# Optimization experiments

Measured on AMD Instinct MI355X. Metric: run time of the kernel, lower is better.

The kernel has to match this reference:

```python
import jax, jax.numpy as jnp
import numpy as np

N_EMBD = 500
BLOCK_SIZE = 256


def _rope(q, k, theta=0.0001):
    # Faithful to the torch code: freq exponent uses the FULL dim C, and the
    # tensor is split into contiguous halves (not interleaved pairs).
    B, T, C = q.shape
    half = C // 2
    i = jnp.arange(half)
    freqs = theta ** (2.0 * (i // 2).astype(q.dtype) / C)  # [half]
    ang = jnp.arange(T, dtype=q.dtype)[:, None] * freqs[None, :]  # [T, half]
    cos_p, sin_p = jnp.cos(ang), jnp.sin(ang)
    q1, q2 = q[..., :half], q[..., half:]
    k1, k2 = k[..., :half], k[..., half:]
    q_rot = jnp.concatenate([q1 * cos_p - q2 * sin_p, q1 * sin_p + q2 * cos_p], axis=-1)
    k_rot = jnp.concatenate([k1 * cos_p - k2 * sin_p, k1 * sin_p + k2 * cos_p], axis=-1)
    return q_rot, k_rot


def setup_inputs() -> dict:
    key = jax.random.key(0)
    k1, k2, k3, k4 = jax.random.split(key, 4)
    B, T = 256, 256
    scale = 1.0 / np.sqrt(N_EMBD)
    x = jax.random.normal(k1, (B, T, N_EMBD), dtype=jnp.float32)
    Wq = jax.random.normal(k2, (N_EMBD, 500), dtype=jnp.float32) * scale
    Wk = jax.random.normal(k3, (N_EMBD, 500), dtype=jnp.float32) * scale
    Wv = jax.random.normal(k4, (N_EMBD, 500), dtype=jnp.float32) * scale
    return {"x": x, "Wq": Wq, "Wk": Wk, "Wv": Wv}


def reference(x, Wq, Wk, Wv):
    B, T, C = x.shape  # C == n_embd == 500
    q = jnp.einsum("btc,ch->bth", x, Wq)
    k = jnp.einsum("btc,ch->bth", x, Wk)
    q, k = _rope(q, k)
    # NOTE: original scales by input-dim C**-0.5 (500), not head_size**-0.5.
    wei = jnp.einsum("bth,bsh->bts", q, k) * (C ** -0.5)
    causal = jnp.tril(jnp.ones((T, T), dtype=bool))
    wei = jnp.where(causal, wei, -jnp.inf)
    wei = jax.nn.softmax(wei, axis=-1)
    # dropout: eval mode (identity) for deterministic reference
    v = jnp.einsum("btc,ch->bth", x, Wv)
    return jnp.einsum("bts,bsh->bth", wei, v)
```

## Files before the change

### kernel.cpp

```cpp
#include <hip/hip_runtime.h>

typedef unsigned short u16;
typedef __attribute__((ext_vector_type(8))) __bf16 bf16x8;
typedef __attribute__((ext_vector_type(4))) float f32x4;

__device__ __forceinline__ float bf2f(u16 u) {
  union { unsigned int i; float f; } v; v.i = ((unsigned int)u) << 16; return v.f;
}
__device__ __forceinline__ u16 f2bf(float f) {
  union { float f; unsigned int i; } v; v.f = f;
  unsigned int u = v.i;
  return (u16)((u + 0x7fffu + ((u >> 16) & 1u)) >> 16);
}
__device__ __forceinline__ void async16(void* lds, const void* g) {
  __builtin_amdgcn_global_load_lds(
      (const __attribute__((address_space(1))) unsigned int*)g,
      (__attribute__((address_space(3))) unsigned int*)lds, 16, 0, 0);
}

__global__ void k_convert_x(const float* __restrict__ x, u16* __restrict__ xb) {
  int idx = blockIdx.x * 256 + threadIdx.x;
  int m = idx >> 6, c0 = (idx & 63) * 8;
  u16 o[8];
  if (c0 < 496) {
    float4 v0 = *(const float4*)(x + (size_t)m * 500 + c0);
    float4 v1 = *(const float4*)(x + (size_t)m * 500 + c0 + 4);
    o[0] = f2bf(v0.x); o[1] = f2bf(v0.y); o[2] = f2bf(v0.z); o[3] = f2bf(v0.w);
    o[4] = f2bf(v1.x); o[5] = f2bf(v1.y); o[6] = f2bf(v1.z); o[7] = f2bf(v1.w);
  } else {
#pragma unroll
    for (int j = 0; j < 8; ++j) {
      int c = c0 + j;
      o[j] = f2bf((c < 500) ? x[(size_t)m * 500 + c] : 0.f);
    }
  }
  *(uint4*)(xb + (size_t)m * 512 + c0) = *(const uint4*)o;
}

__global__ void k_convert_w(const float* __restrict__ Wq, const float* __restrict__ Wk,
                            const float* __restrict__ Wv, u16* __restrict__ Wt) {
  int idx = blockIdx.x * 256 + threadIdx.x;
  int g = idx >> 18;
  int r = idx & 262143;
  int n = r >> 9, k = r & 511;
  const float* W = (g == 0) ? Wq : (g == 1) ? Wk : Wv;
  int orig = (g == 2) ? n : ((n & 1) ? (n >> 1) + 250 : (n >> 1));
  float v = (n < 500 && k < 500) ? W[(size_t)k * 500 + orig] : 0.f;
  Wt[idx] = f2bf(v);
}

__global__ void k_tables(float* __restrict__ cospair, float* __restrict__ sinpair) {
  int t = blockIdx.x, p = threadIdx.x;
  float c = 0.f, s = 0.f;
  if (p < 250) {
    float ex = (float)(2 * (p >> 1)) / 500.0f;
    float fr = powf(1e-4f, ex);
    float ang = (float)t * fr;
    c = cosf(ang); s = sinf(ang);
  }
  cospair[t * 256 + p] = c;
  sinpair[t * 256 + p] = s;
}

__global__ __launch_bounds__(512, 2) void k_gemm_qkv(
    const u16* __restrict__ xb, const u16* __restrict__ Wt,
    const float* __restrict__ cospair, const float* __restrict__ sinpair,
    u16* __restrict__ qb, u16* __restrict__ kb, u16* __restrict__ vT) {
  __shared__ u16 As[2][128][64];
  __shared__ u16 Bs[2][128][64];
  const int tid = threadIdx.x;
  const int lane = tid & 63;
  const int w = tid >> 6;
  const int wm = w >> 2, wn = w & 3;
  const int lrow = lane & 15, lhi = lane >> 4;
  const int sx = lrow & 7;

  int bid = blockIdx.x;
  int wk = (bid & 7) * 192 + (bid >> 3);
  int mg = wk / 12;
  int j12 = wk - mg * 12;
  int g = j12 >> 2, bni = j12 & 3;
  const int bn = bni << 7;
  const int m0 = mg << 9;

  const u16* Ab = xb + (size_t)m0 * 512;
  const u16* Bb = Wt + ((size_t)(g * 512 + bn)) * 512;

#define STAGE(S) { int mt_ = (S) >> 3, t_ = (S) & 7, buf_ = (S) & 1;          \
    _Pragma("unroll")                                                         \
    for (int ld = 0; ld < 2; ++ld) {                                          \
      int gi = ld * 512 + tid;                                                \
      int r_ = gi >> 3, c_ = gi & 7;                                          \
      int so_ = t_ * 64 + ((c_ ^ (r_ & 7)) * 8);                              \
      async16((char*)As + buf_ * 16384 + (size_t)gi * 16,                     \
              Ab + ((size_t)(mt_ * 128 + r_)) * 512 + so_);                   \
      async16((char*)Bs + buf_ * 16384 + (size_t)gi * 16,                     \
              Bb + (size_t)r_ * 512 + so_);                                   \
    } }

#define EPILOGUE(MT) {                                                        \
    int mb = m0 + (MT) * 128;                                                 \
    if (g < 2) {                                                              \
      u16* dst = (g == 0) ? qb : kb;                                          \
      _Pragma("unroll")                                                       \
      for (int mi = 0; mi < 4; ++mi)                                          \
        _Pragma("unroll")                                                     \
        for (int ni = 0; ni < 2; ++ni) {                                      \
          int n = bn + wn * 32 + ni * 16 + lrow;                              \
          int p = n >> 1;                                                     \
          _Pragma("unroll")                                                   \
          for (int jj = 0; jj < 4; ++jj) {                                    \
            int m = mb + wm * 64 + mi * 16 + lhi * 4 + jj;                    \
            float v = acc[mi][ni][jj];                                        \
            float o = __shfl_xor(v, 1, 64);                                   \
            int ti = (m & 255) * 256 + p;                                     \
            float c = cospair[ti], s = sinpair[ti];                           \
            float r = (n & 1) ? (o * s + v * c) : (v * c - o * s);            \
            dst[(size_t)m * 512 + n] = f2bf(r);                               \
          }                                                                   \
        }                                                                     \
    } else {                                                                  \
      _Pragma("unroll")                                                       \
      for (int mi = 0; mi < 4; ++mi)                                          \
        _Pragma("unroll")                                                     \
        for (int ni = 0; ni < 2; ++ni) {                                      \
          int n = bn + wn * 32 + ni * 16 + lrow;                              \
          _Pragma("unroll")                                                   \
          for (int jj = 0; jj < 4; ++jj) {                                    \
            int m = mb + wm * 64 + mi * 16 + lhi * 4 + jj;                    \
            vT[(size_t)(m >> 8) * 131072 + (size_t)n * 256 + (m & 255)] =     \
                f2bf(acc[mi][ni][jj]);                                        \
          }                                                                   \
        }                                                                     \
    } }

  STAGE(0);
  asm volatile("s_waitcnt vmcnt(0)" ::: "memory");
  __builtin_amdgcn_s_barrier();
  asm volatile("" ::: "memory");

  for (int mt = 0; mt < 4; ++mt) {
    f32x4 acc[4][2] = {};
#pragma unroll
    for (int t = 0; t < 8; ++t) {
      const int S = mt * 8 + t;
      if (S + 1 < 32) STAGE(S + 1);
      const u16* Asl = (const u16*)As + (t & 1) * 8192;
      const u16* Bsl = (const u16*)Bs + (t & 1) * 8192;
      bf16x8 a[4][2], bfr[2][2];
#pragma unroll
      for (int mi = 0; mi < 4; ++mi)
#pragma unroll
        for (int kk2 = 0; kk2 < 2; ++kk2)
          a[mi][kk2] = *(const bf16x8*)(Asl + (wm * 64 + mi * 16 + lrow) * 64 +
                                        (((kk2 * 4 + lhi) ^ sx) * 8));
#pragma unroll
      for (int ni = 0; ni < 2; ++ni)
#pragma unroll
        for (int kk2 = 0; kk2 < 2; ++kk2)
          bfr[ni][kk2] = *(const bf16x8*)(Bsl + (wn * 32 + ni * 16 + lrow) * 64 +
                                          (((kk2 * 4 + lhi) ^ sx) * 8));
      __builtin_amdgcn_s_setprio(1);
#pragma unroll
      for (int kk2 = 0; kk2 < 2; ++kk2)
#pragma unroll
        for (int mi = 0; mi < 4; ++mi)
#pragma unroll
          for (int ni = 0; ni < 2; ++ni)
            acc[mi][ni] = __builtin_amdgcn_mfma_f32_16x16x32_bf16(
                a[mi][kk2], bfr[ni][kk2], acc[mi][ni], 0, 0, 0);
      __builtin_amdgcn_s_setprio(0);
      asm volatile("s_waitcnt vmcnt(0)" ::: "memory");
      __builtin_amdgcn_s_barrier();
      asm volatile("" ::: "memory");
    }
    EPILOGUE(mt);
  }
#undef STAGE
#undef EPILOGUE
}

__global__ __launch_bounds__(256) void k_attn(
    const u16* __restrict__ qb, const u16* __restrict__ kb,
    const u16* __restrict__ vT, float* __restrict__ out) {
  __shared__ u16 smem[40960];
  u16* Ring = smem;
  u16* Ps = smem + 24576;

  const int tid = threadIdx.x;
  const int lane = tid & 63;
  const int w = tid >> 6;
  int bid = blockIdx.x;
  int wkk = (bid & 7) * 128 + (bid >> 3);
  const int b = wkk >> 2;
  const int qt = wkk & 3;
  const int t0 = qt * 64;
  const int lrow = lane & 15, lhi = lane >> 4;
  const int sx = lrow & 7;
  const int vxor = (lrow >> 1) & 3;
  const int NT = 4 * (qt + 1);
  const int NTB = 2 * (qt + 1);
  const int NV = 2 * NTB;

  const u16* qrow = qb + ((size_t)(b * 256 + t0 + w * 16 + lrow)) * 512;
  bf16x8 qf[16];
#pragma unroll
  for (int kk = 0; kk < 16; ++kk)
    qf[kk] = *(const bf16x8*)(qrow + kk * 32 + lhi * 8);

#define STAGE_K(ST) {                                                         \
    _Pragma("unroll")                                                         \
    for (int ld = 0; ld < 4; ++ld) {                                          \
      int gi = ld * 256 + tid;                                                \
      int r_ = gi >> 6, c_ = gi & 63;                                         \
      async16((char*)Ring + ((ST) % 3) * 16384 + (size_t)gi * 16,             \
              kb + ((size_t)(b * 256 + (ST) * 16 + r_)) * 512 +               \
                  ((c_ ^ (r_ & 7)) * 8));                                     \
    } }

#define STAGE_V(ST, HH) {                                                     \
    _Pragma("unroll")                                                         \
    for (int ld = 0; ld < 4; ++ld) {                                          \
      int gi = ld * 256 + tid;                                                \
      int r_ = gi >> 2, c_ = gi & 3;                                          \
      async16((char*)Ring + (((ST) * 2 + (HH)) % 3) * 16384 + (size_t)gi * 16,\
              vT + (size_t)b * 131072 + ((size_t)((HH) * 256 + r_)) * 256 +   \
                  (ST) * 32 + ((c_ ^ ((r_ >> 1) & 3)) * 8));                  \
    } }

  f32x4 sa[16] = {};
  STAGE_K(0); STAGE_K(1);
  asm volatile("s_waitcnt vmcnt(4)" ::: "memory");
  __builtin_amdgcn_s_barrier();
  asm volatile("" ::: "memory");
#pragma unroll
  for (int st = 0; st < 16; ++st) {
    if (st < NT) {
      if (st + 2 < NT) STAGE_K(st + 2);
      const u16* Ksl = Ring + (st % 3) * 8192 + lrow * 512;
      __builtin_amdgcn_s_setprio(1);
#pragma unroll
      for (int kk = 0; kk < 16; ++kk) {
        bf16x8 bf = *(const bf16x8*)(Ksl + ((kk * 4 + lhi) ^ sx) * 8);
        sa[st] = __builtin_amdgcn_mfma_f32_16x16x32_bf16(qf[kk], bf, sa[st], 0, 0, 0);
      }
      __builtin_amdgcn_s_setprio(0);
      if (st + 2 < NT)      asm volatile("s_waitcnt vmcnt(4)" ::: "memory");
      else if (st + 1 < NT) asm volatile("s_waitcnt vmcnt(0)" ::: "memory");
      if (st + 1 < NT) {
        __builtin_amdgcn_s_barrier();
        asm volatile("" ::: "memory");
      }
    }
  }

  const float scale = 0.04472135954999579f;
  float rmax[4] = {-1e30f, -1e30f, -1e30f, -1e30f};
#pragma unroll
  for (int n = 0; n < 16; ++n) {
    int s = n * 16 + lrow;
#pragma unroll
    for (int j = 0; j < 4; ++j) {
      int t = t0 + w * 16 + lhi * 4 + j;
      float v = sa[n][j] * scale;
      if (s > t) v = -1e30f;
      sa[n][j] = v;
      rmax[j] = fmaxf(rmax[j], v);
    }
  }
#pragma unroll
  for (int j = 0; j < 4; ++j)
#pragma unroll
    for (int msk = 1; msk < 16; msk <<= 1)
      rmax[j] = fmaxf(rmax[j], __shfl_xor(rmax[j], msk, 64));
  float rsum[4] = {0.f, 0.f, 0.f, 0.f};
#pragma unroll
  for (int n = 0; n < 16; ++n)
#pragma unroll
    for (int j = 0; j < 4; ++j) {
      float p = __expf(sa[n][j] - rmax[j]);
      sa[n][j] = p;
      rsum[j] += p;
    }
#pragma unroll
  for (int j = 0; j < 4; ++j)
#pragma unroll
    for (int msk = 1; msk < 16; msk <<= 1)
      rsum[j] += __shfl_xor(rsum[j], msk, 64);
  float rinv[4];
#pragma unroll
  for (int j = 0; j < 4; ++j) rinv[j] = 1.0f / rsum[j];

#pragma unroll
  for (int n = 0; n < 16; ++n)
#pragma unroll
    for (int j = 0; j < 4; ++j) {
      int s = n * 16 + lrow;
      int trow = w * 16 + lhi * 4 + j;
      int slot = (s >> 3) ^ (trow & 7);
      Ps[trow * 256 + slot * 8 + (s & 7)] = f2bf(sa[n][j] * rinv[j]);
    }

  __syncthreads();

  f32x4 o[2][16] = {};
  STAGE_V(0, 0); STAGE_V(0, 1);
  asm volatile("s_waitcnt vmcnt(4)" ::: "memory");
  __builtin_amdgcn_s_barrier();
  asm volatile("" ::: "memory");
#pragma unroll
  for (int st = 0; st < 8; ++st) {
    if (st < NTB) {
#pragma unroll
      for (int hh = 0; hh < 2; ++hh) {
        const int f = st * 2 + hh;
        if (f + 2 < NV) {
          if (hh == 0) STAGE_V(st + 1, 0) else STAGE_V(st + 1, 1);
        }
        bf16x8 pf = *(const bf16x8*)&Ps[(w * 16 + lrow) * 256 + ((st * 4 + lhi) ^ sx) * 8];
        const u16* Vsl = Ring + (f % 3) * 8192;
        __builtin_amdgcn_s_setprio(1);
#pragma unroll
        for (int ni = 0; ni < 16; ++ni) {
          bf16x8 vf = *(const bf16x8*)(Vsl + (ni * 16 + lrow) * 32 + (lhi ^ vxor) * 8);
          o[hh][ni] = __builtin_amdgcn_mfma_f32_16x16x32_bf16(pf, vf, o[hh][ni], 0, 0, 0);
        }
        __builtin_amdgcn_s_setprio(0);
        if (f + 2 < NV)      asm volatile("s_waitcnt vmcnt(4)" ::: "memory");
        else if (f + 1 < NV) asm volatile("s_waitcnt vmcnt(0)" ::: "memory");
        if (f + 1 < NV) {
          __builtin_amdgcn_s_barrier();
          asm volatile("" ::: "memory");
        }
      }
    }
  }
#undef STAGE_K
#undef STAGE_V

  const int tb = t0 + w * 16;
#pragma unroll
  for (int hh = 0; hh < 2; ++hh)
#pragma unroll
    for (int ni = 0; ni < 16; ++ni) {
      int h = hh * 256 + ni * 16 + lrow;
      if (h < 500) {
#pragma unroll
        for (int j = 0; j < 4; ++j) {
          int t = tb + lhi * 4 + j;
          out[((size_t)(b * 256 + t)) * 500 + h] = o[hh][ni][j];
        }
      }
    }
}

extern "C" void kernel_launch(void* const* d_in, const int* in_sizes, int n_in,
                              void* d_out, int out_size, void* d_ws, size_t ws_size,
                              hipStream_t stream) {
  const float* x  = (const float*)d_in[0];
  const float* Wq = (const float*)d_in[1];
  const float* Wk = (const float*)d_in[2];
  const float* Wv = (const float*)d_in[3];
  float* out = (float*)d_out;

  u16* xb = (u16*)d_ws;
  u16* qb = xb + 33554432;
  u16* kb = qb + 33554432;
  u16* vT = kb + 33554432;
  u16* Wt = vT + 33554432;
  float* cospair = (float*)(Wt + 786432);
  float* sinpair = cospair + 65536;

  k_convert_x<<<16384, 256, 0, stream>>>(x, xb);
  k_convert_w<<<3072, 256, 0, stream>>>(Wq, Wk, Wv, Wt);
  k_tables<<<256, 256, 0, stream>>>(cospair, sinpair);
  k_gemm_qkv<<<1536, 512, 0, stream>>>(xb, Wt, cospair, sinpair, qb, kb, vT);
  k_attn<<<1024, 256, 0, stream>>>(qb, kb, vT, out);
}
```

Before: 371.2 us.

## Restructure QKV GEMM tiles: B from global, 4-stage A pipeline, 256x256 tiles

The QKV projection GEMM now uses 256-row by 256-column block tiles instead of 512x128. The weight (B) fragments are read straight from global memory into registers rather than staged through LDS. The freed LDS becomes a 4-deep ring buffer for A tiles, with three loads kept in flight via partial vmcnt waits. The goal is more MFMA work per barrier and less LDS traffic and synchronisation, at the cost of uncoalesced per-lane global reads of B that depend on cache hits, and more accumulator registers per thread.

```diff
diff --git a/kernel.cpp b/kernel.cpp
--- a/kernel.cpp
+++ b/kernel.cpp
@@ -66,8 +66,7 @@
     const u16* __restrict__ xb, const u16* __restrict__ Wt,
     const float* __restrict__ cospair, const float* __restrict__ sinpair,
     u16* __restrict__ qb, u16* __restrict__ kb, u16* __restrict__ vT) {
-  __shared__ u16 As[2][128][64];
-  __shared__ u16 Bs[2][128][64];
+  __shared__ u16 As[4][128][64];
   const int tid = threadIdx.x;
   const int lane = tid & 63;
   const int w = tid >> 6;
@@ -77,25 +76,47 @@
 
   int bid = blockIdx.x;
   int wk = (bid & 7) * 192 + (bid >> 3);
-  int mg = wk / 12;
-  int j12 = wk - mg * 12;
-  int g = j12 >> 2, bni = j12 & 3;
-  const int bn = bni << 7;
-  const int m0 = mg << 9;
+  int mg = wk / 6;
+  int j6 = wk - mg * 6;
+  int g = j6 >> 1, bni = j6 & 1;
+  const int bn = bni << 8;
+  const int m0 = mg << 8;
 
   const u16* Ab = xb + (size_t)m0 * 512;
-  const u16* Bb = Wt + ((size_t)(g * 512 + bn)) * 512;
-
-#define STAGE(S) { int mt_ = (S) >> 3, t_ = (S) & 7, buf_ = (S) & 1;          \
+  const u16* Bl = Wt + ((size_t)(g * 512 + bn + wn * 64) + lrow) * 512 + lhi * 8;
+
+#define STAGE(S) { int mt_ = (S) >> 3, t_ = (S) & 7, buf_ = (S) & 3;          \
     _Pragma("unroll")                                                         \
     for (int ld = 0; ld < 2; ++ld) {                                          \
       int gi = ld * 512 + tid;                                                \
       int r_ = gi >> 3, c_ = gi & 7;                                          \
-      int so_ = t_ * 64 + ((c_ ^ (r_ & 7)) * 8);                              \
       async16((char*)As + buf_ * 16384 + (size_t)gi * 16,                     \
-              Ab + ((size_t)(mt_ * 128 + r_)) * 512 + so_);                   \
-      async16((char*)Bs + buf_ * 16384 + (size_t)gi * 16,                     \
-              Bb + (size_t)r_ * 512 + so_);                                   \
+              Ab + ((size_t)(mt_ * 128 + r_)) * 512 + t_ * 64 +               \
+                  ((c_ ^ (r_ & 7)) * 8));                                     \
+    } }
+
+#define COMPUTE(S) {                                                          \
+    const u16* Asl = (const u16*)As + ((S) & 3) * 8192;                       \
+    const int t_ = (S) & 7;                                                   \
+    _Pragma("unroll")                                                         \
+    for (int kk2 = 0; kk2 < 2; ++kk2) {                                       \
+      bf16x8 a[4], bfr[4];                                                    \
+      _Pragma("unroll")                                                       \
+      for (int mi = 0; mi < 4; ++mi)                                          \
+        a[mi] = *(const bf16x8*)(Asl + (wm * 64 + mi * 16 + lrow) * 64 +      \
+                                 (((kk2 * 4 + lhi) ^ sx) * 8));               \
+      _Pragma("unroll")                                                       \
+      for (int ni = 0; ni < 4; ++ni)                                          \
+        bfr[ni] = *(const bf16x8*)(Bl + (size_t)ni * 16 * 512 + t_ * 64 +     \
+                                   kk2 * 32);                                 \
+      __builtin_amdgcn_s_setprio(1);                                          \
+      _Pragma("unroll")                                                       \
+      for (int mi = 0; mi < 4; ++mi)                                          \
+        _Pragma("unroll")                                                     \
+        for (int ni = 0; ni < 4; ++ni)                                        \
+          acc[mi][ni] = __builtin_amdgcn_mfma_f32_16x16x32_bf16(              \
+              a[mi], bfr[ni], acc[mi][ni], 0, 0, 0);                          \
+      __builtin_amdgcn_s_setprio(0);                                          \
     } }
 
 #define EPILOGUE(MT) {                                                        \
@@ -105,8 +126,8 @@
       _Pragma("unroll")                                                       \
       for (int mi = 0; mi < 4; ++mi)                                          \
         _Pragma("unroll")                                                     \
-        for (int ni = 0; ni < 2; ++ni) {                                      \
-          int n = bn + wn * 32 + ni * 16 + lrow;                              \
+        for (int ni = 0; ni < 4; ++ni) {                                      \
+          int n = bn + wn * 64 + ni * 16 + lrow;                              \
           int p = n >> 1;                                                     \
           _Pragma("unroll")                                                   \
           for (int jj = 0; jj < 4; ++jj) {                                    \
@@ -123,8 +144,8 @@
       _Pragma("unroll")                                                       \
       for (int mi = 0; mi < 4; ++mi)                                          \
         _Pragma("unroll")                                                     \
-        for (int ni = 0; ni < 2; ++ni) {                                      \
-          int n = bn + wn * 32 + ni * 16 + lrow;                              \
+        for (int ni = 0; ni < 4; ++ni) {                                      \
+          int n = bn + wn * 64 + ni * 16 + lrow;                              \
           _Pragma("unroll")                                                   \
           for (int jj = 0; jj < 4; ++jj) {                                    \
             int m = mb + wm * 64 + mi * 16 + lhi * 4 + jj;                    \
@@ -134,49 +155,31 @@
         }                                                                     \
     } }
 
-  STAGE(0);
-  asm volatile("s_waitcnt vmcnt(0)" ::: "memory");
+  STAGE(0); STAGE(1); STAGE(2);
+  asm volatile("s_waitcnt vmcnt(4)" ::: "memory");
   __builtin_amdgcn_s_barrier();
   asm volatile("" ::: "memory");
 
-  for (int mt = 0; mt < 4; ++mt) {
-    f32x4 acc[4][2] = {};
+#pragma unroll
+  for (int mt = 0; mt < 2; ++mt) {
+    f32x4 acc[4][4] = {};
 #pragma unroll
     for (int t = 0; t < 8; ++t) {
       const int S = mt * 8 + t;
-      if (S + 1 < 32) STAGE(S + 1);
-      const u16* Asl = (const u16*)As + (t & 1) * 8192;
-      const u16* Bsl = (const u16*)Bs + (t & 1) * 8192;
-      bf16x8 a[4][2], bfr[2][2];
-#pragma unroll
-      for (int mi = 0; mi < 4; ++mi)
-#pragma unroll
-        for (int kk2 = 0; kk2 < 2; ++kk2)
-          a[mi][kk2] = *(const bf16x8*)(Asl + (wm * 64 + mi * 16 + lrow) * 64 +
-                                        (((kk2 * 4 + lhi) ^ sx) * 8));
-#pragma unroll
-      for (int ni = 0; ni < 2; ++ni)
-#pragma unroll
-        for (int kk2 = 0; kk2 < 2; ++kk2)
-          bfr[ni][kk2] = *(const bf16x8*)(Bsl + (wn * 32 + ni * 16 + lrow) * 64 +
-                                          (((kk2 * 4 + lhi) ^ sx) * 8));
-      __builtin_amdgcn_s_setprio(1);
-#pragma unroll
-      for (int kk2 = 0; kk2 < 2; ++kk2)
-#pragma unroll
-        for (int mi = 0; mi < 4; ++mi)
-#pragma unroll
-          for (int ni = 0; ni < 2; ++ni)
-            acc[mi][ni] = __builtin_amdgcn_mfma_f32_16x16x32_bf16(
-                a[mi][kk2], bfr[ni][kk2], acc[mi][ni], 0, 0, 0);
-      __builtin_amdgcn_s_setprio(0);
-      asm volatile("s_waitcnt vmcnt(0)" ::: "memory");
-      __builtin_amdgcn_s_barrier();
-      asm volatile("" ::: "memory");
+      if (S + 3 < 16) STAGE(S + 3);
+      COMPUTE(S);
+      if (S < 13)       asm volatile("s_waitcnt vmcnt(4)" ::: "memory");
+      else if (S == 13) asm volatile("s_waitcnt vmcnt(2)" ::: "memory");
+      else if (S == 14) asm volatile("s_waitcnt vmcnt(0)" ::: "memory");
+      if (S < 15) {
+        __builtin_amdgcn_s_barrier();
+        asm volatile("" ::: "memory");
+      }
     }
     EPILOGUE(mt);
   }
 #undef STAGE
+#undef COMPUTE
 #undef EPILOGUE
 }
 
```

Result: slower. 436.5 us (+17.6%).
